# Performance work log

Hardware: AMD Instinct MI355X
Metric: run time of the kernel (lower is better)

## Reference

```python
import jax, jax.numpy as jnp
import numpy as np
from jax import lax


def _lstm_layer(x, Wih, Whh, bih, bhh):
    # x: [B, T, D_in]; PyTorch gate order: i, f, g, o. Returns all hidden states [B, T, H].
    B = x.shape[0]
    H = Whh.shape[1]
    bias = bih + bhh
    # Precompute input projections for all timesteps: [T, B, 4H]
    xg = jnp.einsum('btd,gd->tbg', x, Wih) + bias

    def step(carry, xg_t):
        h, c = carry
        gates = xg_t + h @ Whh.T  # [B, 4H]
        i, f, g, o = jnp.split(gates, 4, axis=-1)
        i = jax.nn.sigmoid(i)
        f = jax.nn.sigmoid(f)
        g = jnp.tanh(g)
        o = jax.nn.sigmoid(o)
        c = f * c + i * g
        h = o * jnp.tanh(c)
        return (h, c), h

    h0 = jnp.zeros((B, H), dtype=x.dtype)
    c0 = jnp.zeros((B, H), dtype=x.dtype)
    (_, _), hs = lax.scan(step, (h0, c0), xg)  # hs: [T, B, H]
    return hs.transpose(1, 0, 2)


def setup_inputs() -> dict:
    key = jax.random.key(0)
    ks = jax.random.split(key, 13)
    B, T, D = 4096, 128, 32
    H1, H2 = 64, 32
    s = lambda n: 1.0 / np.sqrt(n)
    return {
        'x': jax.random.normal(ks[0], (B, T, D), jnp.float32),
        'Wih1': jax.random.uniform(ks[1], (4 * H1, D), jnp.float32, -s(H1), s(H1)),
        'Whh1': jax.random.uniform(ks[2], (4 * H1, H1), jnp.float32, -s(H1), s(H1)),
        'bih1': jax.random.uniform(ks[3], (4 * H1,), jnp.float32, -s(H1), s(H1)),
        'bhh1': jax.random.uniform(ks[4], (4 * H1,), jnp.float32, -s(H1), s(H1)),
        'Wih2': jax.random.uniform(ks[5], (4 * H2, H1), jnp.float32, -s(H2), s(H2)),
        'Whh2': jax.random.uniform(ks[6], (4 * H2, H2), jnp.float32, -s(H2), s(H2)),
        'bih2': jax.random.uniform(ks[7], (4 * H2,), jnp.float32, -s(H2), s(H2)),
        'bhh2': jax.random.uniform(ks[8], (4 * H2,), jnp.float32, -s(H2), s(H2)),
        'fc1_w': jax.random.uniform(ks[9], (16, H2), jnp.float32, -s(H2), s(H2)),
        'fc1_b': jax.random.uniform(ks[10], (16,), jnp.float32, -s(H2), s(H2)),
        'fc2_w': jax.random.uniform(ks[11], (1, 16), jnp.float32, -0.25, 0.25),
        'fc2_b': jax.random.uniform(ks[12], (1,), jnp.float32, -0.25, 0.25),
    }


def reference(x, Wih1, Whh1, bih1, bhh1, Wih2, Whh2, bih2, bhh2, fc1_w, fc1_b, fc2_w, fc2_b):
    out = _lstm_layer(x, Wih1, Whh1, bih1, bhh1)        # [B, T, H1]; dropout = identity (eval)
    out = _lstm_layer(out, Wih2, Whh2, bih2, bhh2)       # [B, T, H2]
    last = out[:, -1, :]                                  # [B, H2]
    h = jax.nn.relu(last @ fc1_w.T + fc1_b)               # [B, 16]
    return h @ fc2_w.T + fc2_b                            # [B, 1]
```

## Files before the change

### kernel.cpp

```cpp
#include <hip/hip_runtime.h>


constexpr int Tt      = 128;
constexpr int NB      = 16;
constexpr int THREADS = 512;

struct __align__(16) Smem {
  float w2t[96][132];
  float scr[48][256];
  float h1t[2][64][20];
  float h2t[2][32][20];
  float xs [2][32][20];
};

static_assert(sizeof(Smem) <= 160 * 1024, "LDS overflow");

__device__ __forceinline__ float frcp(float x)   { return __builtin_amdgcn_rcpf(x); }
__device__ __forceinline__ float fsig(float x)   { return frcp(1.0f + __expf(-x)); }
__device__ __forceinline__ float ftanh_(float x) { return 1.0f - 2.0f * frcp(1.0f + __expf(2.0f * x)); }

template<int P>
__device__ __forceinline__ float swz(float v) {
  return __int_as_float(__builtin_amdgcn_ds_swizzle(__float_as_int(v), P));
}

__global__ __launch_bounds__(THREADS, 2)
void lstm_fused(const float* __restrict__ x,
                const float* __restrict__ Wih1, const float* __restrict__ Whh1,
                const float* __restrict__ bih1, const float* __restrict__ bhh1,
                const float* __restrict__ Wih2, const float* __restrict__ Whh2,
                const float* __restrict__ bih2, const float* __restrict__ bhh2,
                const float* __restrict__ fc1w, const float* __restrict__ fc1b,
                const float* __restrict__ fc2w, const float* __restrict__ fc2b,
                float* __restrict__ out)
{
  __shared__ Smem s;
  const int tid = threadIdx.x;
  const int wv  = tid >> 6;
  const int l   = tid & 63;
  const int b0  = blockIdx.x * NB;

  const int ks  = l & 7;
  const int bh  = (l >> 3) & 1;
  const int pq  = l >> 4;
  const int up  = wv * 4 + pq;
  const int u2  = wv * 4 + pq;
  const int bh8 = bh * 8;
  const int myb = bh8 + ks;

  for (int e = tid; e < 128 * 64; e += THREADS) {
    int r = e >> 6, k = e & 63;
    s.w2t[k][(r & 31) * 4 + (r >> 5)] = Wih2[e];
  }
  for (int e = tid; e < 128 * 32; e += THREADS) {
    int r = e >> 5, k = e & 31;
    s.w2t[64 + k][(r & 31) * 4 + (r >> 5)] = Whh2[e];
  }
  for (int e = tid; e < 256 * 32; e += THREADS) {
    int r = e >> 5, k = e & 31;
    s.scr[k][(r & 63) * 4 + (r >> 6)] = Wih1[e];
  }
  for (int e = tid; e < 256 * 16; e += THREADS) {
    int r = e >> 4, kc = e & 15;
    s.scr[32 + kc][(r & 63) * 4 + (r >> 6)] = Whh1[r * 64 + kc];
  }
  __syncthreads();

  float w1[12][8];
#pragma unroll
  for (int j = 0; j < 6; ++j) {
    int k = ks + 8 * j;
    float4 a4 = *(const float4*)&s.scr[k][up * 8];
    float4 b4 = *(const float4*)&s.scr[k][up * 8 + 4];
    w1[j][0] = a4.x; w1[j][1] = a4.y; w1[j][2] = a4.z; w1[j][3] = a4.w;
    w1[j][4] = b4.x; w1[j][5] = b4.y; w1[j][6] = b4.z; w1[j][7] = b4.w;
  }
  __syncthreads();

  for (int e = tid; e < 256 * 64; e += THREADS) {
    int r = e >> 6, k = e & 63;
    if (k >= 16) s.scr[k - 16][(r & 63) * 4 + (r >> 6)] = Whh1[e];
  }
  for (int e = tid; e < 64 * 20; e += THREADS) (&s.h1t[0][0][0])[e] = 0.0f;
  for (int e = tid; e < 32 * 20; e += THREADS) (&s.h2t[0][0][0])[e] = 0.0f;
  __syncthreads();

#pragma unroll
  for (int j = 6; j < 12; ++j) {
    int k = ks + 8 * j;
    float4 a4 = *(const float4*)&s.scr[k - 48][up * 8];
    float4 b4 = *(const float4*)&s.scr[k - 48][up * 8 + 4];
    w1[j][0] = a4.x; w1[j][1] = a4.y; w1[j][2] = a4.z; w1[j][3] = a4.w;
    w1[j][4] = b4.x; w1[j][5] = b4.y; w1[j][6] = b4.z; w1[j][7] = b4.w;
  }

  float bias1[8], bias2[4];
#pragma unroll
  for (int uu = 0; uu < 2; ++uu)
#pragma unroll
    for (int g = 0; g < 4; ++g) {
      int u = 2 * up + uu;
      bias1[uu * 4 + g] = bih1[g * 64 + u] + bhh1[g * 64 + u];
    }
#pragma unroll
  for (int g = 0; g < 4; ++g) bias2[g] = bih2[g * 32 + u2] + bhh2[g * 32 + u2];

  const int    xb   = tid >> 5;
  const int    xd   = tid & 31;
  const float* xptr = x + (size_t)(b0 + xb) * (Tt * 32) + xd;
  s.xs[0][xd][xb] = xptr[0];

  float c1[2] = {0.0f, 0.0f};
  float c2    = 0.0f;

  const bool k0b = (ks & 1) != 0;
  const bool k1b = (ks & 2) != 0;
  const bool k2b = (ks & 4) != 0;

  __syncthreads();

#pragma unroll 1
  for (int t = 0; t < Tt; ++t) {
    const int c = t & 1, n = c ^ 1;

    float xpre = 0.0f;
    if (t + 1 < Tt) xpre = xptr[(size_t)(t + 1) * 32];

    float a[8][8];
#pragma unroll
    for (int g = 0; g < 8; ++g)
#pragma unroll
      for (int b = 0; b < 8; ++b) a[g][b] = 0.0f;

#pragma unroll
    for (int j = 0; j < 12; ++j) {
      const float* hrow = (j < 4) ? &s.xs[c][ks + 8 * j][0]
                                  : &s.h1t[c][ks + 8 * j - 32][0];
      float4 h0 = *(const float4*)(hrow + bh8);
      float4 h1 = *(const float4*)(hrow + bh8 + 4);
      float hv[8] = {h0.x, h0.y, h0.z, h0.w, h1.x, h1.y, h1.z, h1.w};
#pragma unroll
      for (int g = 0; g < 8; ++g)
#pragma unroll
        for (int b = 0; b < 8; ++b)
          a[g][b] = fmaf(w1[j][g], hv[b], a[g][b]);
    }

    float tot[8];
#pragma unroll
    for (int g = 0; g < 8; ++g) {
      float r1[4], r2[2];
#pragma unroll
      for (int i = 0; i < 4; ++i) {
        float snd  = k0b ? a[g][2 * i]     : a[g][2 * i + 1];
        float kept = k0b ? a[g][2 * i + 1] : a[g][2 * i];
        r1[i] = kept + swz<0x041F>(snd);
      }
#pragma unroll
      for (int i = 0; i < 2; ++i) {
        float snd  = k1b ? r1[2 * i]     : r1[2 * i + 1];
        float kept = k1b ? r1[2 * i + 1] : r1[2 * i];
        r2[i] = kept + swz<0x081F>(snd);
      }
      float snd  = k2b ? r2[0] : r2[1];
      float kept = k2b ? r2[1] : r2[0];
      tot[g] = kept + swz<0x101F>(snd);
    }

#pragma unroll
    for (int uu = 0; uu < 2; ++uu) {
      float iv = fsig  (tot[4 * uu + 0] + bias1[4 * uu + 0]);
      float fv = fsig  (tot[4 * uu + 1] + bias1[4 * uu + 1]);
      float gv = ftanh_(tot[4 * uu + 2] + bias1[4 * uu + 2]);
      float ov = fsig  (tot[4 * uu + 3] + bias1[4 * uu + 3]);
      c1[uu] = fv * c1[uu] + iv * gv;
      s.h1t[n][2 * up + uu][myb] = ov * ftanh_(c1[uu]);
    }
    __syncthreads();

    if (t + 1 < Tt) s.xs[n][xd][xb] = xpre;

    float a2[4][8];
#pragma unroll
    for (int g = 0; g < 4; ++g)
#pragma unroll
      for (int b = 0; b < 8; ++b) a2[g][b] = 0.0f;

#pragma unroll
    for (int j = 0; j < 12; ++j) {
      const int k = ks + 8 * j;
      const float* hrow = (j < 8) ? &s.h1t[n][k][0] : &s.h2t[c][k - 64][0];
      float4 wv4 = *(const float4*)&s.w2t[k][u2 * 4];
      float4 h0  = *(const float4*)(hrow + bh8);
      float4 h1  = *(const float4*)(hrow + bh8 + 4);
      float wvv[4] = {wv4.x, wv4.y, wv4.z, wv4.w};
      float hv[8]  = {h0.x, h0.y, h0.z, h0.w, h1.x, h1.y, h1.z, h1.w};
#pragma unroll
      for (int g = 0; g < 4; ++g)
#pragma unroll
        for (int b = 0; b < 8; ++b)
          a2[g][b] = fmaf(wvv[g], hv[b], a2[g][b]);
    }

    float tot2[4];
#pragma unroll
    for (int g = 0; g < 4; ++g) {
      float r1[4], r2[2];
#pragma unroll
      for (int i = 0; i < 4; ++i) {
        float snd  = k0b ? a2[g][2 * i]     : a2[g][2 * i + 1];
        float kept = k0b ? a2[g][2 * i + 1] : a2[g][2 * i];
        r1[i] = kept + swz<0x041F>(snd);
      }
#pragma unroll
      for (int i = 0; i < 2; ++i) {
        float snd  = k1b ? r1[2 * i]     : r1[2 * i + 1];
        float kept = k1b ? r1[2 * i + 1] : r1[2 * i];
        r2[i] = kept + swz<0x081F>(snd);
      }
      float snd  = k2b ? r2[0] : r2[1];
      float kept = k2b ? r2[1] : r2[0];
      tot2[g] = kept + swz<0x101F>(snd);
    }

    {
      float iv = fsig  (tot2[0] + bias2[0]);
      float fv = fsig  (tot2[1] + bias2[1]);
      float gv = ftanh_(tot2[2] + bias2[2]);
      float ov = fsig  (tot2[3] + bias2[3]);
      c2 = fv * c2 + iv * gv;
      s.h2t[n][u2][myb] = ov * ftanh_(c2);
    }
    __syncthreads();
  }

  float* fc1out = &s.h2t[1][0][0];
  if (tid < 256) {
    const int fb = tid >> 4, fu = tid & 15;
    float sacc = fc1b[fu];
#pragma unroll
    for (int k = 0; k < 32; ++k)
      sacc = fmaf(fc1w[fu * 32 + k], s.h2t[0][k][fb], sacc);
    fc1out[fb * 16 + fu] = fmaxf(sacc, 0.0f);
  }
  __syncthreads();
  if (tid < 16) {
    float o = fc2b[0];
#pragma unroll
    for (int u = 0; u < 16; ++u) o = fmaf(fc2w[u], fc1out[tid * 16 + u], o);
    out[b0 + tid] = o;
  }
}

extern "C" void kernel_launch(void* const* d_in, const int* in_sizes, int n_in,
                              void* d_out, int out_size, void* d_ws, size_t ws_size,
                              hipStream_t stream) {
  const float* x    = (const float*)d_in[0];
  const float* Wih1 = (const float*)d_in[1];
  const float* Whh1 = (const float*)d_in[2];
  const float* bih1 = (const float*)d_in[3];
  const float* bhh1 = (const float*)d_in[4];
  const float* Wih2 = (const float*)d_in[5];
  const float* Whh2 = (const float*)d_in[6];
  const float* bih2 = (const float*)d_in[7];
  const float* bhh2 = (const float*)d_in[8];
  const float* fc1w = (const float*)d_in[9];
  const float* fc1b = (const float*)d_in[10];
  const float* fc2w = (const float*)d_in[11];
  const float* fc2b = (const float*)d_in[12];
  float* out = (float*)d_out;

  hipLaunchKernelGGL(lstm_fused, dim3(256), dim3(THREADS), 0, stream,
                     x, Wih1, Whh1, bih1, bhh1,
                     Wih2, Whh2, bih2, bhh2,
                     fc1w, fc1b, fc2w, fc2b, out);
}
```

Before: 681.2 us.

## Halve batch per block and keep both LSTM layers' weights in registers

Blocks shrink from 16 batch rows and 512 threads to 8 rows and 256 threads, with twice as many blocks so two blocks share a CU. The thread-to-work mapping is reorganized. Layer-1 lanes now split the reduction over 4 k-slices and end up owning 2 batch rows each. Layer-2 weights are loaded into registers through a staged float4 LDS scratch buffer instead of being read from LDS every step. The goal is cheaper barriers within each smaller block and no per-step LDS weight traffic, at the cost of higher register use and one block's latency no longer overlapping within a single large workgroup.

```diff
diff --git a/kernel.cpp b/kernel.cpp
--- a/kernel.cpp
+++ b/kernel.cpp
@@ -2,18 +2,17 @@
 
 
 constexpr int Tt      = 128;
-constexpr int NB      = 16;
-constexpr int THREADS = 512;
+constexpr int NB      = 8;
+constexpr int THREADS = 256;
 
 struct __align__(16) Smem {
-  float w2t[96][132];
-  float scr[48][256];
-  float h1t[2][64][20];
-  float h2t[2][32][20];
-  float xs [2][32][20];
+  float scr[8192];
+  float h1t[2][64][12];
+  float h2t[2][32][12];
+  float xs [2][32][12];
 };
 
-static_assert(sizeof(Smem) <= 160 * 1024, "LDS overflow");
+static_assert(sizeof(Smem) <= 80 * 1024, "need 2 blocks/CU");
 
 __device__ __forceinline__ float frcp(float x)   { return __builtin_amdgcn_rcpf(x); }
 __device__ __forceinline__ float fsig(float x)   { return frcp(1.0f + __expf(-x)); }
@@ -36,74 +35,74 @@
 {
   __shared__ Smem s;
   const int tid = threadIdx.x;
-  const int wv  = tid >> 6;
-  const int l   = tid & 63;
   const int b0  = blockIdx.x * NB;
 
-  const int ks  = l & 7;
-  const int bh  = (l >> 3) & 1;
-  const int pq  = l >> 4;
-  const int up  = wv * 4 + pq;
-  const int u2  = wv * 4 + pq;
-  const int bh8 = bh * 8;
-  const int myb = bh8 + ks;
-
-  for (int e = tid; e < 128 * 64; e += THREADS) {
-    int r = e >> 6, k = e & 63;
-    s.w2t[k][(r & 31) * 4 + (r >> 5)] = Wih2[e];
-  }
-  for (int e = tid; e < 128 * 32; e += THREADS) {
-    int r = e >> 5, k = e & 31;
-    s.w2t[64 + k][(r & 31) * 4 + (r >> 5)] = Whh2[e];
-  }
-  for (int e = tid; e < 256 * 32; e += THREADS) {
-    int r = e >> 5, k = e & 31;
-    s.scr[k][(r & 63) * 4 + (r >> 6)] = Wih1[e];
-  }
-  for (int e = tid; e < 256 * 16; e += THREADS) {
-    int r = e >> 4, kc = e & 15;
-    s.scr[32 + kc][(r & 63) * 4 + (r >> 6)] = Whh1[r * 64 + kc];
-  }
-  __syncthreads();
-
-  float w1[12][8];
-#pragma unroll
-  for (int j = 0; j < 6; ++j) {
-    int k = ks + 8 * j;
-    float4 a4 = *(const float4*)&s.scr[k][up * 8];
-    float4 b4 = *(const float4*)&s.scr[k][up * 8 + 4];
-    w1[j][0] = a4.x; w1[j][1] = a4.y; w1[j][2] = a4.z; w1[j][3] = a4.w;
-    w1[j][4] = b4.x; w1[j][5] = b4.y; w1[j][6] = b4.z; w1[j][7] = b4.w;
-  }
-  __syncthreads();
-
-  for (int e = tid; e < 256 * 64; e += THREADS) {
-    int r = e >> 6, k = e & 63;
-    if (k >= 16) s.scr[k - 16][(r & 63) * 4 + (r >> 6)] = Whh1[e];
-  }
-  for (int e = tid; e < 64 * 20; e += THREADS) (&s.h1t[0][0][0])[e] = 0.0f;
-  for (int e = tid; e < 32 * 20; e += THREADS) (&s.h2t[0][0][0])[e] = 0.0f;
-  __syncthreads();
-
-#pragma unroll
-  for (int j = 6; j < 12; ++j) {
-    int k = ks + 8 * j;
-    float4 a4 = *(const float4*)&s.scr[k - 48][up * 8];
-    float4 b4 = *(const float4*)&s.scr[k - 48][up * 8 + 4];
-    w1[j][0] = a4.x; w1[j][1] = a4.y; w1[j][2] = a4.z; w1[j][3] = a4.w;
-    w1[j][4] = b4.x; w1[j][5] = b4.y; w1[j][6] = b4.z; w1[j][7] = b4.w;
-  }
-
-  float bias1[8], bias2[4];
-#pragma unroll
-  for (int uu = 0; uu < 2; ++uu)
-#pragma unroll
-    for (int g = 0; g < 4; ++g) {
-      int u = 2 * up + uu;
-      bias1[uu * 4 + g] = bih1[g * 64 + u] + bhh1[g * 64 + u];
-    }
-#pragma unroll
-  for (int g = 0; g < 4; ++g) bias2[g] = bih2[g * 32 + u2] + bhh2[g * 32 + u2];
+  const int ks1 = tid & 3;
+  const int u1  = tid >> 2;
+  const int ks2 = tid & 7;
+  const int u2  = tid >> 3;
+
+  float w1[24][4];
+  float w2[12][4];
+
+  auto stage = [&](const float* g, int n) {
+    for (int e = tid * 4; e < n; e += THREADS * 4)
+      *(float4*)&s.scr[e] = *(const float4*)&g[e];
+  };
+
+  stage(Wih1, 8192);
+  __syncthreads();
+#pragma unroll
+  for (int j = 0; j < 8; ++j)
+#pragma unroll
+    for (int g = 0; g < 4; ++g)
+      w1[j][g] = s.scr[(g * 64 + u1) * 32 + ks1 + 4 * j];
+  __syncthreads();
+
+  stage(Whh1, 8192);
+  __syncthreads();
+#pragma unroll
+  for (int j = 8; j < 24; ++j)
+#pragma unroll
+    for (int g = 0; g < 2; ++g)
+      w1[j][g] = s.scr[(g * 64 + u1) * 64 + ks1 + 4 * (j - 8)];
+  __syncthreads();
+
+  stage(Whh1 + 8192, 8192);
+  __syncthreads();
+#pragma unroll
+  for (int j = 8; j < 24; ++j)
+#pragma unroll
+    for (int g = 2; g < 4; ++g)
+      w1[j][g] = s.scr[((g - 2) * 64 + u1) * 64 + ks1 + 4 * (j - 8)];
+  __syncthreads();
+
+  stage(Wih2, 8192);
+  __syncthreads();
+#pragma unroll
+  for (int j = 0; j < 8; ++j)
+#pragma unroll
+    for (int g = 0; g < 4; ++g)
+      w2[j][g] = s.scr[(g * 32 + u2) * 64 + ks2 + 8 * j];
+  __syncthreads();
+
+  stage(Whh2, 4096);
+  __syncthreads();
+#pragma unroll
+  for (int j = 8; j < 12; ++j)
+#pragma unroll
+    for (int g = 0; g < 4; ++g)
+      w2[j][g] = s.scr[(g * 32 + u2) * 32 + ks2 + 8 * (j - 8)];
+
+  float bias1[4], bias2[4];
+#pragma unroll
+  for (int g = 0; g < 4; ++g) {
+    bias1[g] = bih1[g * 64 + u1] + bhh1[g * 64 + u1];
+    bias2[g] = bih2[g * 32 + u2] + bhh2[g * 32 + u2];
+  }
+
+  for (int e = tid; e < 64 * 12; e += THREADS) (&s.h1t[0][0][0])[e] = 0.0f;
+  for (int e = tid; e < 32 * 12; e += THREADS) (&s.h2t[0][0][0])[e] = 0.0f;
 
   const int    xb   = tid >> 5;
   const int    xd   = tid & 31;
@@ -113,9 +112,11 @@
   float c1[2] = {0.0f, 0.0f};
   float c2    = 0.0f;
 
-  const bool k0b = (ks & 1) != 0;
-  const bool k1b = (ks & 2) != 0;
-  const bool k2b = (ks & 4) != 0;
+  const bool sA = (ks1 & 1) != 0;
+  const bool sB = (ks1 & 2) != 0;
+  const bool t0 = (ks2 & 1) != 0;
+  const bool t1 = (ks2 & 2) != 0;
+  const bool t2 = (ks2 & 4) != 0;
 
   __syncthreads();
 
@@ -126,100 +127,96 @@
     float xpre = 0.0f;
     if (t + 1 < Tt) xpre = xptr[(size_t)(t + 1) * 32];
 
-    float a[8][8];
-#pragma unroll
-    for (int g = 0; g < 8; ++g)
+    float a[4][8];
+#pragma unroll
+    for (int g = 0; g < 4; ++g)
 #pragma unroll
       for (int b = 0; b < 8; ++b) a[g][b] = 0.0f;
 
 #pragma unroll
-    for (int j = 0; j < 12; ++j) {
-      const float* hrow = (j < 4) ? &s.xs[c][ks + 8 * j][0]
-                                  : &s.h1t[c][ks + 8 * j - 32][0];
-      float4 h0 = *(const float4*)(hrow + bh8);
-      float4 h1 = *(const float4*)(hrow + bh8 + 4);
+    for (int j = 0; j < 24; ++j) {
+      const float* row = (j < 8) ? &s.xs[c][ks1 + 4 * j][0]
+                                 : &s.h1t[c][ks1 + 4 * j - 32][0];
+      float4 h0 = *(const float4*)&row[0];
+      float4 h1 = *(const float4*)&row[4];
       float hv[8] = {h0.x, h0.y, h0.z, h0.w, h1.x, h1.y, h1.z, h1.w};
 #pragma unroll
-      for (int g = 0; g < 8; ++g)
+      for (int g = 0; g < 4; ++g)
 #pragma unroll
         for (int b = 0; b < 8; ++b)
           a[g][b] = fmaf(w1[j][g], hv[b], a[g][b]);
     }
 
-    float tot[8];
-#pragma unroll
-    for (int g = 0; g < 8; ++g) {
-      float r1[4], r2[2];
+    float tot[4][2];
+#pragma unroll
+    for (int g = 0; g < 4; ++g) {
+      float r1[4];
 #pragma unroll
       for (int i = 0; i < 4; ++i) {
-        float snd  = k0b ? a[g][2 * i]     : a[g][2 * i + 1];
-        float kept = k0b ? a[g][2 * i + 1] : a[g][2 * i];
+        float snd  = sA ? a[g][2 * i]     : a[g][2 * i + 1];
+        float kept = sA ? a[g][2 * i + 1] : a[g][2 * i];
         r1[i] = kept + swz<0x041F>(snd);
       }
 #pragma unroll
       for (int i = 0; i < 2; ++i) {
-        float snd  = k1b ? r1[2 * i]     : r1[2 * i + 1];
-        float kept = k1b ? r1[2 * i + 1] : r1[2 * i];
+        float snd  = sB ? r1[2 * i]     : r1[2 * i + 1];
+        float kept = sB ? r1[2 * i + 1] : r1[2 * i];
+        tot[g][i] = kept + swz<0x081F>(snd);
+      }
+    }
+
+#pragma unroll
+    for (int bb = 0; bb < 2; ++bb) {
+      float iv = fsig  (tot[0][bb] + bias1[0]);
+      float fv = fsig  (tot[1][bb] + bias1[1]);
+      float gv = ftanh_(tot[2][bb] + bias1[2]);
+      float ov = fsig  (tot[3][bb] + bias1[3]);
+      c1[bb] = fv * c1[bb] + iv * gv;
+      s.h1t[n][u1][ks1 + 4 * bb] = ov * ftanh_(c1[bb]);
+    }
+    __syncthreads();
+
+    if (t + 1 < Tt) s.xs[n][xd][xb] = xpre;
+
+    float a2[4][8];
+#pragma unroll
+    for (int g = 0; g < 4; ++g)
+#pragma unroll
+      for (int b = 0; b < 8; ++b) a2[g][b] = 0.0f;
+
+#pragma unroll
+    for (int j = 0; j < 12; ++j) {
+      const int k = ks2 + 8 * j;
+      const float* row = (j < 8) ? &s.h1t[n][k][0] : &s.h2t[c][k - 64][0];
+      float4 h0 = *(const float4*)&row[0];
+      float4 h1 = *(const float4*)&row[4];
+      float hv[8] = {h0.x, h0.y, h0.z, h0.w, h1.x, h1.y, h1.z, h1.w};
+#pragma unroll
+      for (int g = 0; g < 4; ++g)
+#pragma unroll
+        for (int b = 0; b < 8; ++b)
+          a2[g][b] = fmaf(w2[j][g], hv[b], a2[g][b]);
+    }
+
+    float tot2[4];
+#pragma unroll
+    for (int g = 0; g < 4; ++g) {
+      float r1[4];
+#pragma unroll
+      for (int i = 0; i < 4; ++i) {
+        float snd  = t0 ? a2[g][2 * i]     : a2[g][2 * i + 1];
+        float kept = t0 ? a2[g][2 * i + 1] : a2[g][2 * i];
+        r1[i] = kept + swz<0x041F>(snd);
+      }
+      float r2[2];
+#pragma unroll
+      for (int i = 0; i < 2; ++i) {
+        float snd  = t1 ? r1[2 * i]     : r1[2 * i + 1];
+        float kept = t1 ? r1[2 * i + 1] : r1[2 * i];
         r2[i] = kept + swz<0x081F>(snd);
       }
-      float snd  = k2b ? r2[0] : r2[1];
-      float kept = k2b ? r2[1] : r2[0];
-      tot[g] = kept + swz<0x101F>(snd);
-    }
-
-#pragma unroll
-    for (int uu = 0; uu < 2; ++uu) {
-      float iv = fsig  (tot[4 * uu + 0] + bias1[4 * uu + 0]);
-      float fv = fsig  (tot[4 * uu + 1] + bias1[4 * uu + 1]);
-      float gv = ftanh_(tot[4 * uu + 2] + bias1[4 * uu + 2]);
-      float ov = fsig  (tot[4 * uu + 3] + bias1[4 * uu + 3]);
-      c1[uu] = fv * c1[uu] + iv * gv;
-      s.h1t[n][2 * up + uu][myb] = ov * ftanh_(c1[uu]);
-    }
-    __syncthreads();
-
-    if (t + 1 < Tt) s.xs[n][xd][xb] = xpre;
-
-    float a2[4][8];
-#pragma unroll
-    for (int g = 0; g < 4; ++g)
-#pragma unroll
-      for (int b = 0; b < 8; ++b) a2[g][b] = 0.0f;
-
-#pragma unroll
-    for (int j = 0; j < 12; ++j) {
-      const int k = ks + 8 * j;
-      const float* hrow = (j < 8) ? &s.h1t[n][k][0] : &s.h2t[c][k - 64][0];
-      float4 wv4 = *(const float4*)&s.w2t[k][u2 * 4];
-      float4 h0  = *(const float4*)(hrow + bh8);
-      float4 h1  = *(const float4*)(hrow + bh8 + 4);
-      float wvv[4] = {wv4.x, wv4.y, wv4.z, wv4.w};
-      float hv[8]  = {h0.x, h0.y, h0.z, h0.w, h1.x, h1.y, h1.z, h1.w};
-#pragma unroll
-      for (int g = 0; g < 4; ++g)
-#pragma unroll
-        for (int b = 0; b < 8; ++b)
-          a2[g][b] = fmaf(wvv[g], hv[b], a2[g][b]);
-    }
-
-    float tot2[4];
-#pragma unroll
-    for (int g = 0; g < 4; ++g) {
-      float r1[4], r2[2];
-#pragma unroll
-      for (int i = 0; i < 4; ++i) {
-        float snd  = k0b ? a2[g][2 * i]     : a2[g][2 * i + 1];
-        float kept = k0b ? a2[g][2 * i + 1] : a2[g][2 * i];
-        r1[i] = kept + swz<0x041F>(snd);
-      }
-#pragma unroll
-      for (int i = 0; i < 2; ++i) {
-        float snd  = k1b ? r1[2 * i]     : r1[2 * i + 1];
-        float kept = k1b ? r1[2 * i + 1] : r1[2 * i];
-        r2[i] = kept + swz<0x081F>(snd);
-      }
-      float snd  = k2b ? r2[0] : r2[1];
-      float kept = k2b ? r2[1] : r2[0];
+      float snd  = t2 ? r2[0] : r2[1];
+      float kept = t2 ? r2[1] : r2[0];
       tot2[g] = kept + swz<0x101F>(snd);
     }
 
@@ -229,13 +226,13 @@
       float gv = ftanh_(tot2[2] + bias2[2]);
       float ov = fsig  (tot2[3] + bias2[3]);
       c2 = fv * c2 + iv * gv;
-      s.h2t[n][u2][myb] = ov * ftanh_(c2);
+      s.h2t[n][u2][ks2] = ov * ftanh_(c2);
     }
     __syncthreads();
   }
 
-  float* fc1out = &s.h2t[1][0][0];
-  if (tid < 256) {
+  float* fc1out = s.scr;
+  if (tid < 128) {
     const int fb = tid >> 4, fu = tid & 15;
     float sacc = fc1b[fu];
 #pragma unroll
@@ -244,7 +241,7 @@
     fc1out[fb * 16 + fu] = fmaxf(sacc, 0.0f);
   }
   __syncthreads();
-  if (tid < 16) {
+  if (tid < NB) {
     float o = fc2b[0];
 #pragma unroll
     for (int u = 0; u < 16; ++u) o = fmaf(fc2w[u], fc1out[tid * 16 + u], o);
@@ -270,7 +267,7 @@
   const float* fc2b = (const float*)d_in[12];
   float* out = (float*)d_out;
 
-  hipLaunchKernelGGL(lstm_fused, dim3(256), dim3(THREADS), 0, stream,
+  hipLaunchKernelGGL(lstm_fused, dim3(4096 / NB), dim3(THREADS), 0, stream,
                      x, Wih1, Whh1, bih1, bhh1,
                      Wih2, Whh2, bih2, bhh2,
                      fc1w, fc1b, fc2w, fc2b, out);
```

New measurement: 675.7 us. About the same (-0.8%).
